# Kernel optimization log

Hardware: AMD Instinct MI355X
Metric: run time of the kernel (lower is better)

## Reference

```python
import math
import jax, jax.numpy as jnp
from jax import lax
import numpy as np

HIDDEN = 128
KQ_CH = HIDDEN * 3  # 384
H, W = 48, 64
N = 4


def _conv(x, w, pad, dil):
    # NCHW conv, OIHW weights, stride 1
    return lax.conv_general_dilated(
        x, w, window_strides=(1, 1),
        padding=[(pad, pad), (pad, pad)],
        rhs_dilation=(dil, dil),
        dimension_numbers=("NCHW", "OIHW", "NCHW"))


def _lrelu(x):
    return jnp.where(x >= 0, x, 0.2 * x)


def setup_inputs() -> dict:
    key = jax.random.key(0)
    ks = jax.random.split(key, 7)
    s = 0.05
    return {
        "k": jax.random.normal(ks[0], (N, KQ_CH, H, W), jnp.float32),
        "q": jax.random.normal(ks[1], (N, KQ_CH, H, W), jnp.float32),
        "v": jax.random.normal(ks[2], (N, HIDDEN, H, W), jnp.float32),
        "w_value": jax.random.normal(ks[3], (HIDDEN, HIDDEN, 1, 1), jnp.float32) * s,
        "w_out": jax.random.normal(ks[4], (HIDDEN, HIDDEN, 3, 3), jnp.float32) * s,
        "w_ff1": jax.random.normal(ks[5], (HIDDEN, HIDDEN, 3, 3), jnp.float32) * s,
        "w_ff2": jax.random.normal(ks[6], (HIDDEN, HIDDEN, 3, 3), jnp.float32) * s,
    }


def reference(k, q, v, w_value, w_out, w_ff1, w_ff2):
    n, c, h, w = k.shape  # c = kq_channels
    hw = h * w
    # value embedding: 1x1 conv
    val = _conv(v, w_value, 0, 1)  # [n, hidden, h, w]
    kf = k.reshape(n, c, hw)
    qf = q.reshape(n, c, hw)
    # scores[n, key_pos, query_pos] = k^T q / sqrt(c)
    scores = jnp.einsum("nck,ncq->nkq", kf, qf) / math.sqrt(c)
    # softmax over key positions (torch dim=-2)
    p_attn = jax.nn.softmax(scores, axis=1)  # [n, hw, hw]
    # p_val = value @ p_attn
    p_val = jnp.einsum("ndk,nkq->ndq", val.reshape(n, -1, hw), p_attn)
    p_val = p_val.reshape(v.shape)
    # residual update with output_linear (conv3x3 + LeakyReLU)
    v2 = v + _lrelu(_conv(p_val, w_out, 1, 1))
    # dilated-conv feed forward with residual
    ff = _lrelu(_conv(_lrelu(_conv(v2, w_ff1, 2, 2)), w_ff2, 1, 1))
    return v2 + ff
```

## Files before the change

### kernel.cpp

```cpp
#include <hip/hip_runtime.h>

#define NB  4
#define CKQ 384
#define DH  128
#define HH  48
#define WW  64
#define HW  3072

#define NSPLIT 16
#define KSEG  (HW / NSPLIT)
#define BQ 128
#define BK 32
#define VSP 40
#define PTS 40
#define XROW 136

typedef short bf16x8 __attribute__((ext_vector_type(8)));
typedef short b16x4  __attribute__((ext_vector_type(4)));
typedef float f32x4  __attribute__((ext_vector_type(4)));
typedef long  i64;
typedef long  i64x2 __attribute__((ext_vector_type(2)));
typedef unsigned short u16;
typedef unsigned int   u32;
typedef unsigned char  u8;
typedef unsigned long long u64;

__device__ __forceinline__ float b2f(u16 u){
  union { u32 i; float f; } x; x.i = ((u32)u) << 16; return x.f;
}
__device__ __forceinline__ u16 f2b(float f){
  union { float f; u32 i; } x; x.f = f;
  u32 r = (x.i + 0x7fffu + ((x.i >> 16) & 1u)) >> 16;
  return (u16)r;
}
__device__ __forceinline__ u8 f2f8(float f){
  return (u8)(__builtin_amdgcn_cvt_pk_fp8_f32(f, f, 0, false) & 0xff);
}

__global__ __launch_bounds__(256)
void tcast8(const float* __restrict__ kin, const float* __restrict__ qin,
            u8* __restrict__ kt8, u8* __restrict__ qt8){
  __shared__ u8 T[64][392];
  const int yy = blockIdx.y;
  const float* in = (yy < NB) ? kin : qin;
  u8* out         = (yy < NB) ? kt8 : qt8;
  const int n  = yy & (NB - 1);
  const int p0 = blockIdx.x * 64;
  const int tx = threadIdx.x & 63;
  const int ty = threadIdx.x >> 6;
  const float* ib = in + (size_t)n * CKQ * HW + p0;
  #pragma unroll 4
  for (int c = ty; c < CKQ; c += 4)
    T[tx][c] = f2f8(ib[(size_t)c * HW + tx]);
  __syncthreads();
  u8* ob = out + ((size_t)n * HW + p0) * CKQ;
  #pragma unroll
  for (int it = 0; it < 12; ++it){
    int ch  = it * 256 + threadIdx.x;
    int row = ch / 48;
    int g   = ch - row * 48;
    *(u64*)(ob + (size_t)row * CKQ + g * 8) = *(const u64*)&T[row][g * 8];
  }
}

__global__ __launch_bounds__(256)
void wprep3(const float* __restrict__ w0, const float* __restrict__ w1,
            const float* __restrict__ w2, u16* __restrict__ o0,
            u16* __restrict__ o1, u16* __restrict__ o2){
  const float* w = (blockIdx.y == 0) ? w0 : (blockIdx.y == 1) ? w1 : w2;
  u16* wt        = (blockIdx.y == 0) ? o0 : (blockIdx.y == 1) ? o1 : o2;
  int g    = blockIdx.x * 256 + threadIdx.x;
  int fid  = g >> 6;
  int lane = g & 63;
  int l15  = lane & 15, quad = lane >> 4;
  int tap  = fid >> 5;
  int cst  = (fid >> 3) & 3;
  int dt   = fid & 7;
  int d    = dt * 16 + l15;
  u16* dst = wt + (size_t)fid * 512 + lane * 8;
  #pragma unroll
  for (int e = 0; e < 8; ++e){
    int c = cst * 32 + quad * 8 + e;
    dst[e] = f2b(w[((size_t)d * DH + c) * 9 + tap]);
  }
}

__global__ __launch_bounds__(256)
void val_embed8(const float* __restrict__ v, const float* __restrict__ wv,
                u8* __restrict__ val8){
  int p  = blockIdx.x * 256 + threadIdx.x;
  int d0 = blockIdx.y * 4;
  int n  = blockIdx.z;
  const float* vb = v + (size_t)n * DH * HW;
  float a0 = 0.f, a1 = 0.f, a2 = 0.f, a3 = 0.f;
  for (int c = 0; c < DH; ++c){
    float vv = vb[c * HW + p];
    a0 += wv[(d0 + 0) * DH + c] * vv;
    a1 += wv[(d0 + 1) * DH + c] * vv;
    a2 += wv[(d0 + 2) * DH + c] * vv;
    a3 += wv[(d0 + 3) * DH + c] * vv;
  }
  u8* ob = val8 + (size_t)n * DH * HW;
  ob[(d0 + 0) * HW + p] = f2f8(a0);
  ob[(d0 + 1) * HW + p] = f2f8(a1);
  ob[(d0 + 2) * HW + p] = f2f8(a2);
  ob[(d0 + 3) * HW + p] = f2f8(a3);
}

__global__ __launch_bounds__(256, 3)
void attn8(const u8* __restrict__ kt, const u8* __restrict__ qt,
           const u8* __restrict__ val, u16* __restrict__ outp,
           float* __restrict__ lsum){
  __shared__ u8 Ks[BK * CKQ];
  __shared__ u8 Vs[DH * VSP];
  __shared__ u8 Pt[BQ * PTS];

  const int tid  = threadIdx.x;
  const int wv   = tid >> 6;
  const int lane = tid & 63;
  const int quad = lane >> 4;
  const int l15  = lane & 15;
  const int n    = blockIdx.z;
  const int seg  = blockIdx.y;
  const int j0   = blockIdx.x * BQ;
  const int jra  = wv * 32 + l15;
  const int jrb  = jra + 16;
  const int ja   = j0 + jra;
  const int jb   = j0 + jrb;

  const u8* qrowa = qt + ((size_t)n * HW + ja) * CKQ;
  const u8* qrowb = qt + ((size_t)n * HW + jb) * CKQ;
  i64 qfa[12], qfb[12];
  #pragma unroll
  for (int cs = 0; cs < 12; ++cs){
    qfa[cs] = *(const i64*)&qrowa[cs * 32 + quad * 8];
    qfb[cs] = *(const i64*)&qrowb[cs * 32 + quad * 8];
  }

  const f32x4 zero = {0.f, 0.f, 0.f, 0.f};
  f32x4 oa[8], obacc[8];
  #pragma unroll
  for (int i = 0; i < 8; ++i){ oa[i] = zero; obacc[i] = zero; }
  float la = 0.f, lbv = 0.f;

  const u8* ktb = kt  + (size_t)n * CKQ * HW;
  const u8* vb  = val + (size_t)n * DH * HW;
  const float scale = 0.05103103630798287f;

  for (int it = 0; it < KSEG / BK; ++it){
    const int i0 = seg * KSEG + it * BK;
    for (int idx = tid; idx < BK * 24; idx += 256){
      int i  = idx / 24;
      int g2 = idx % 24;
      i64x2 dv = *(const i64x2*)&ktb[(size_t)(i0 + i) * CKQ + g2 * 16];
      int g0 = 2 * g2, g1 = g0 + 1;
      int gs0 = (g0 & ~7) | ((g0 ^ i) & 7);
      int gs1 = (g1 & ~7) | ((g1 ^ i) & 7);
      *(i64*)&Ks[i * CKQ + gs0 * 8] = dv[0];
      *(i64*)&Ks[i * CKQ + gs1 * 8] = dv[1];
    }
    for (int idx = tid; idx < DH * 4; idx += 256){
      int dd = idx >> 2;
      int c8 = idx & 3;
      *(i64*)&Vs[dd * VSP + c8 * 8] = *(const i64*)&vb[(size_t)dd * HW + i0 + c8 * 8];
    }
    __syncthreads();

    f32x4 s0a = zero, s1a = zero, s0b = zero, s1b = zero;
    #pragma unroll
    for (int cs = 0; cs < 12; ++cs){
      int g  = 4 * cs + quad;
      int gs = (g & ~7) | ((g ^ l15) & 7);
      i64 a0 = *(const i64*)&Ks[l15 * CKQ + gs * 8];
      i64 a1 = *(const i64*)&Ks[(16 + l15) * CKQ + gs * 8];
      s0a = __builtin_amdgcn_mfma_f32_16x16x32_fp8_fp8(a0, qfa[cs], s0a, 0, 0, 0);
      s1a = __builtin_amdgcn_mfma_f32_16x16x32_fp8_fp8(a1, qfa[cs], s1a, 0, 0, 0);
      s0b = __builtin_amdgcn_mfma_f32_16x16x32_fp8_fp8(a0, qfb[cs], s0b, 0, 0, 0);
      s1b = __builtin_amdgcn_mfma_f32_16x16x32_fp8_fp8(a1, qfb[cs], s1b, 0, 0, 0);
    }

    float pa[8], pb[8]; float tsa = 0.f, tsb = 0.f;
    #pragma unroll
    for (int r = 0; r < 4; ++r){
      pa[r]     = __expf(s0a[r] * scale);
      pa[4 + r] = __expf(s1a[r] * scale);
      pb[r]     = __expf(s0b[r] * scale);
      pb[4 + r] = __expf(s1b[r] * scale);
    }
    #pragma unroll
    for (int i = 0; i < 8; ++i){ tsa += pa[i]; tsb += pb[i]; }
    la += tsa; lbv += tsb;

    u32 wa0 = __builtin_amdgcn_cvt_pk_fp8_f32(pa[0], pa[1], 0, false);
    wa0     = __builtin_amdgcn_cvt_pk_fp8_f32(pa[2], pa[3], wa0, true);
    u32 wa1 = __builtin_amdgcn_cvt_pk_fp8_f32(pa[4], pa[5], 0, false);
    wa1     = __builtin_amdgcn_cvt_pk_fp8_f32(pa[6], pa[7], wa1, true);
    u32 wb0 = __builtin_amdgcn_cvt_pk_fp8_f32(pb[0], pb[1], 0, false);
    wb0     = __builtin_amdgcn_cvt_pk_fp8_f32(pb[2], pb[3], wb0, true);
    u32 wb1 = __builtin_amdgcn_cvt_pk_fp8_f32(pb[4], pb[5], 0, false);
    wb1     = __builtin_amdgcn_cvt_pk_fp8_f32(pb[6], pb[7], wb1, true);
    *(u32*)&Pt[jra * PTS + quad * 4]      = wa0;
    *(u32*)&Pt[jra * PTS + 16 + quad * 4] = wa1;
    *(u32*)&Pt[jrb * PTS + quad * 4]      = wb0;
    *(u32*)&Pt[jrb * PTS + 16 + quad * 4] = wb1;
    __builtin_amdgcn_wave_barrier();

    i64 bpa = *(const i64*)&Pt[jra * PTS + quad * 8];
    i64 bpb = *(const i64*)&Pt[jrb * PTS + quad * 8];
    #pragma unroll
    for (int dt = 0; dt < 8; ++dt){
      i64 av = *(const i64*)&Vs[(dt * 16 + l15) * VSP + quad * 8];
      oa[dt]    = __builtin_amdgcn_mfma_f32_16x16x32_fp8_fp8(av, bpa, oa[dt], 0, 0, 0);
      obacc[dt] = __builtin_amdgcn_mfma_f32_16x16x32_fp8_fp8(av, bpb, obacc[dt], 0, 0, 0);
    }
    __syncthreads();
  }

  la  += __shfl_xor(la, 16);  la  += __shfl_xor(la, 32);
  lbv += __shfl_xor(lbv, 16); lbv += __shfl_xor(lbv, 32);

  u16* obp = outp + ((size_t)(seg * NB + n) * HW) * DH;
  #pragma unroll
  for (int dt = 0; dt < 8; ++dt){
    b16x4 pka = { (short)f2b(oa[dt][0]), (short)f2b(oa[dt][1]),
                  (short)f2b(oa[dt][2]), (short)f2b(oa[dt][3]) };
    b16x4 pkb = { (short)f2b(obacc[dt][0]), (short)f2b(obacc[dt][1]),
                  (short)f2b(obacc[dt][2]), (short)f2b(obacc[dt][3]) };
    *(b16x4*)&obp[(size_t)ja * DH + dt * 16 + quad * 4] = pka;
    *(b16x4*)&obp[(size_t)jb * DH + dt * 16 + quad * 4] = pkb;
  }
  if (quad == 0){
    lsum[(size_t)(seg * NB + n) * HW + ja] = la;
    lsum[(size_t)(seg * NB + n) * HW + jb] = lbv;
  }
}

__global__ __launch_bounds__(256)
void combine(const u16* __restrict__ ob, const float* __restrict__ lb,
             u16* __restrict__ pval_t){
  size_t flat = (size_t)blockIdx.x * 256 + threadIdx.x;
  int d = (int)(flat & 127);
  size_t nj = flat >> 7;
  int j = (int)(nj % HW);
  int n = (int)(nj / HW);
  float acc = 0.f, ls = 0.f;
  #pragma unroll
  for (int s = 0; s < NSPLIT; ++s){
    acc += b2f(ob[((size_t)(s * NB + n) * HW + j) * DH + d]);
    ls  += lb[(size_t)(s * NB + n) * HW + j];
  }
  pval_t[flat] = f2b(acc / ls);
}

template<int DIL, int RESM, int OUTM>
__global__ __launch_bounds__(256, 3)
void mconv(const u16* __restrict__ in_t, const u16* __restrict__ wtf,
           const void* __restrict__ res, void* __restrict__ out){
  __shared__ u16 Xs[3 * 64 * XROW];

  const int tid  = threadIdx.x;
  const int w    = tid >> 6;
  const int lane = tid & 63;
  const int quad = lane >> 4;
  const int l15  = lane & 15;
  const int n    = blockIdx.z;
  const int y    = blockIdx.x;
  const int by   = blockIdx.y;
  const int xw   = w * 16;

  const bf16x8 bz8 = {0,0,0,0,0,0,0,0};
  #pragma unroll
  for (int yi = 0; yi < 3; ++yi){
    int ysrc = y + (yi - 1) * DIL;
    bool ok = (unsigned)ysrc < (unsigned)HH;
    #pragma unroll
    for (int pass = 0; pass < 4; ++pass){
      int ch = pass * 256 + tid;
      int x  = ch >> 4;
      int g  = ch & 15;
      bf16x8 v = bz8;
      if (ok)
        v = *(const bf16x8*)&in_t[((size_t)n * HW + ysrc * WW + x) * DH + g * 8];
      *(bf16x8*)&Xs[(yi * 64 + x) * XROW + g * 8] = v;
    }
  }
  __syncthreads();

  f32x4 acc[2];
  acc[0] = (f32x4){0.f, 0.f, 0.f, 0.f};
  acc[1] = (f32x4){0.f, 0.f, 0.f, 0.f};

  #pragma unroll
  for (int tap = 0; tap < 9; ++tap){
    const int yi = tap / 3;
    const int dx = (tap % 3 - 1) * DIL;
    const int xp = xw + l15 + dx;
    const bool vx = (unsigned)xp < (unsigned)WW;
    const int xc = vx ? xp : 0;
    const u16* xrow = &Xs[(yi * 64 + xc) * XROW];
    #pragma unroll
    for (int cst = 0; cst < 4; ++cst){
      bf16x8 bf = bz8;
      if (vx) bf = *(const bf16x8*)&xrow[cst * 32 + quad * 8];
      #pragma unroll
      for (int dt = 0; dt < 2; ++dt){
        int fid = (tap * 4 + cst) * 8 + by * 2 + dt;
        bf16x8 af = *(const bf16x8*)&wtf[(size_t)fid * 512 + lane * 8];
        acc[dt] = __builtin_amdgcn_mfma_f32_16x16x32_bf16(af, bf, acc[dt], 0, 0, 0);
      }
    }
  }

  const int p = y * WW + xw + l15;
  #pragma unroll
  for (int dt = 0; dt < 2; ++dt){
    const int d0q = by * 32 + dt * 16 + quad * 4;
    float v4[4];
    #pragma unroll
    for (int r = 0; r < 4; ++r){
      float vv = acc[dt][r];
      vv = (vv >= 0.f) ? vv : 0.2f * vv;
      if (RESM == 1)
        vv += ((const float*)res)[((size_t)n * DH + d0q + r) * HW + p];
      v4[r] = vv;
    }
    if (RESM == 2){
      b16x4 rv = *(const b16x4*)&((const u16*)res)[((size_t)n * HW + p) * DH + d0q];
      #pragma unroll
      for (int r = 0; r < 4; ++r) v4[r] += b2f((u16)rv[r]);
    }
    if (OUTM == 0){
      b16x4 pk = { (short)f2b(v4[0]), (short)f2b(v4[1]),
                   (short)f2b(v4[2]), (short)f2b(v4[3]) };
      *(b16x4*)&((u16*)out)[((size_t)n * HW + p) * DH + d0q] = pk;
    } else {
      #pragma unroll
      for (int r = 0; r < 4; ++r)
        ((float*)out)[((size_t)n * DH + d0q + r) * HW + p] = v4[r];
    }
  }
}

extern "C" void kernel_launch(void* const* d_in, const int* in_sizes, int n_in,
                              void* d_out, int out_size, void* d_ws, size_t ws_size,
                              hipStream_t stream){
  const float* k    = (const float*)d_in[0];
  const float* q    = (const float*)d_in[1];
  const float* v    = (const float*)d_in[2];
  const float* wv   = (const float*)d_in[3];
  const float* wout = (const float*)d_in[4];
  const float* wff1 = (const float*)d_in[5];
  const float* wff2 = (const float*)d_in[6];
  float* out = (float*)d_out;

  const size_t TEN  = (size_t)NB * DH * HW;
  const size_t KTEN = (size_t)NB * CKQ * HW;
  const size_t WT   = (size_t)9 * DH * DH;
  u8*  kt8    = (u8*)d_ws;
  u8*  qt8    = kt8 + KTEN;
  u8*  val8   = qt8 + KTEN;
  u16* wt1    = (u16*)(val8 + TEN);
  u16* wt2    = wt1 + WT;
  u16* wt3    = wt2 + WT;
  u16* pval_t = wt3 + WT;
  u16* v2_t   = pval_t + TEN;
  u16* tmid_t = v2_t + TEN;
  u16* ob     = tmid_t + TEN;
  float* lb   = (float*)(ob + (size_t)NSPLIT * TEN);

  tcast8    <<<dim3(48, 2 * NB), 256, 0, stream>>>(k, q, kt8, qt8);
  wprep3    <<<dim3(72, 3), 256, 0, stream>>>(wout, wff1, wff2, wt1, wt2, wt3);
  val_embed8<<<dim3(12, 32, NB), 256, 0, stream>>>(v, wv, val8);
  attn8     <<<dim3(HW / BQ, NSPLIT, NB), 256, 0, stream>>>(kt8, qt8, val8, ob, lb);
  combine   <<<dim3((unsigned)(TEN / 256)), 256, 0, stream>>>(ob, lb, pval_t);
  mconv<1, 1, 0><<<dim3(48, 4, NB), 256, 0, stream>>>(pval_t, wt1, (const void*)v,    (void*)v2_t);
  mconv<2, 0, 0><<<dim3(48, 4, NB), 256, 0, stream>>>(v2_t,   wt2, (const void*)nullptr, (void*)tmid_t);
  mconv<1, 2, 1><<<dim3(48, 4, NB), 256, 0, stream>>>(tmid_t, wt3, (const void*)v2_t, (void*)out);
}
```

Measured before the change: 231.9 us.

## Merge prep kernels into one launch and split attention launch in two halves

Fuses the fp8 transpose-cast, weight repacking and value embedding into one prep kernel dispatched by block index, cutting two launches. The value embedding now computes 16 output channels per thread instead of 4, so each input load is reused across more channels. The attention kernel now takes a segment offset and is launched twice with half the split each. That halves the grid per launch but adds one launch, plausibly to affect scheduling or cache behaviour.

```diff
diff --git a/kernel.cpp b/kernel.cpp
--- a/kernel.cpp
+++ b/kernel.cpp
@@ -38,79 +38,86 @@
 }
 
 __global__ __launch_bounds__(256)
-void tcast8(const float* __restrict__ kin, const float* __restrict__ qin,
-            u8* __restrict__ kt8, u8* __restrict__ qt8){
+void prep(const float* __restrict__ k, const float* __restrict__ q,
+          const float* __restrict__ v, const float* __restrict__ wv,
+          const float* __restrict__ w0, const float* __restrict__ w1,
+          const float* __restrict__ w2,
+          u8* __restrict__ kt8, u8* __restrict__ qt8, u8* __restrict__ val8,
+          u16* __restrict__ o0, u16* __restrict__ o1, u16* __restrict__ o2){
   __shared__ u8 T[64][392];
-  const int yy = blockIdx.y;
-  const float* in = (yy < NB) ? kin : qin;
-  u8* out         = (yy < NB) ? kt8 : qt8;
-  const int n  = yy & (NB - 1);
-  const int p0 = blockIdx.x * 64;
-  const int tx = threadIdx.x & 63;
-  const int ty = threadIdx.x >> 6;
-  const float* ib = in + (size_t)n * CKQ * HW + p0;
-  #pragma unroll 4
-  for (int c = ty; c < CKQ; c += 4)
-    T[tx][c] = f2f8(ib[(size_t)c * HW + tx]);
-  __syncthreads();
-  u8* ob = out + ((size_t)n * HW + p0) * CKQ;
-  #pragma unroll
-  for (int it = 0; it < 12; ++it){
-    int ch  = it * 256 + threadIdx.x;
-    int row = ch / 48;
-    int g   = ch - row * 48;
-    *(u64*)(ob + (size_t)row * CKQ + g * 8) = *(const u64*)&T[row][g * 8];
-  }
-}
-
-__global__ __launch_bounds__(256)
-void wprep3(const float* __restrict__ w0, const float* __restrict__ w1,
-            const float* __restrict__ w2, u16* __restrict__ o0,
-            u16* __restrict__ o1, u16* __restrict__ o2){
-  const float* w = (blockIdx.y == 0) ? w0 : (blockIdx.y == 1) ? w1 : w2;
-  u16* wt        = (blockIdx.y == 0) ? o0 : (blockIdx.y == 1) ? o1 : o2;
-  int g    = blockIdx.x * 256 + threadIdx.x;
-  int fid  = g >> 6;
-  int lane = g & 63;
-  int l15  = lane & 15, quad = lane >> 4;
-  int tap  = fid >> 5;
-  int cst  = (fid >> 3) & 3;
-  int dt   = fid & 7;
-  int d    = dt * 16 + l15;
-  u16* dst = wt + (size_t)fid * 512 + lane * 8;
-  #pragma unroll
-  for (int e = 0; e < 8; ++e){
-    int c = cst * 32 + quad * 8 + e;
-    dst[e] = f2b(w[((size_t)d * DH + c) * 9 + tap]);
-  }
-}
-
-__global__ __launch_bounds__(256)
-void val_embed8(const float* __restrict__ v, const float* __restrict__ wv,
-                u8* __restrict__ val8){
-  int p  = blockIdx.x * 256 + threadIdx.x;
-  int d0 = blockIdx.y * 4;
-  int n  = blockIdx.z;
-  const float* vb = v + (size_t)n * DH * HW;
-  float a0 = 0.f, a1 = 0.f, a2 = 0.f, a3 = 0.f;
-  for (int c = 0; c < DH; ++c){
-    float vv = vb[c * HW + p];
-    a0 += wv[(d0 + 0) * DH + c] * vv;
-    a1 += wv[(d0 + 1) * DH + c] * vv;
-    a2 += wv[(d0 + 2) * DH + c] * vv;
-    a3 += wv[(d0 + 3) * DH + c] * vv;
-  }
-  u8* ob = val8 + (size_t)n * DH * HW;
-  ob[(d0 + 0) * HW + p] = f2f8(a0);
-  ob[(d0 + 1) * HW + p] = f2f8(a1);
-  ob[(d0 + 2) * HW + p] = f2f8(a2);
-  ob[(d0 + 3) * HW + p] = f2f8(a3);
+  const int b   = blockIdx.x;
+  const int tid = threadIdx.x;
+
+  if (b < 384){
+    const int yy = b / 48;
+    const int bx = b % 48;
+    const float* in = (yy < NB) ? k : q;
+    u8* outp        = (yy < NB) ? kt8 : qt8;
+    const int n  = yy & (NB - 1);
+    const int p0 = bx * 64;
+    const int tx = tid & 63;
+    const int ty = tid >> 6;
+    const float* ib = in + (size_t)n * CKQ * HW + p0;
+    #pragma unroll 4
+    for (int c = ty; c < CKQ; c += 4)
+      T[tx][c] = f2f8(ib[(size_t)c * HW + tx]);
+    __syncthreads();
+    u8* ob = outp + ((size_t)n * HW + p0) * CKQ;
+    #pragma unroll
+    for (int it = 0; it < 12; ++it){
+      int ch  = it * 256 + tid;
+      int row = ch / 48;
+      int g   = ch - row * 48;
+      *(u64*)(ob + (size_t)row * CKQ + g * 8) = *(const u64*)&T[row][g * 8];
+    }
+  } else if (b < 600){
+    const int bb = b - 384;
+    const int bx = bb % 72;
+    const int wy = bb / 72;
+    const float* w = (wy == 0) ? w0 : (wy == 1) ? w1 : w2;
+    u16* wt        = (wy == 0) ? o0 : (wy == 1) ? o1 : o2;
+    int g    = bx * 256 + tid;
+    int fid  = g >> 6;
+    int lane = g & 63;
+    int l15  = lane & 15, quad = lane >> 4;
+    int tap  = fid >> 5;
+    int cst  = (fid >> 3) & 3;
+    int dt   = fid & 7;
+    int d    = dt * 16 + l15;
+    u16* dst = wt + (size_t)fid * 512 + lane * 8;
+    #pragma unroll
+    for (int e = 0; e < 8; ++e){
+      int c = cst * 32 + quad * 8 + e;
+      dst[e] = f2b(w[((size_t)d * DH + c) * 9 + tap]);
+    }
+  } else {
+    const int bb = b - 600;
+    const int px = bb % 12;
+    const int db = (bb / 12) & 7;
+    const int n  = bb / 96;
+    const int p  = px * 256 + tid;
+    const int d0 = db * 16;
+    const float* vb = v + (size_t)n * DH * HW;
+    float acc[16];
+    #pragma unroll
+    for (int dd = 0; dd < 16; ++dd) acc[dd] = 0.f;
+    for (int c = 0; c < DH; ++c){
+      float vv = vb[(size_t)c * HW + p];
+      #pragma unroll
+      for (int dd = 0; dd < 16; ++dd)
+        acc[dd] += wv[(d0 + dd) * DH + c] * vv;
+    }
+    u8* ob = val8 + (size_t)n * DH * HW;
+    #pragma unroll
+    for (int dd = 0; dd < 16; ++dd)
+      ob[(size_t)(d0 + dd) * HW + p] = f2f8(acc[dd]);
+  }
 }
 
 __global__ __launch_bounds__(256, 3)
 void attn8(const u8* __restrict__ kt, const u8* __restrict__ qt,
            const u8* __restrict__ val, u16* __restrict__ outp,
-           float* __restrict__ lsum){
+           float* __restrict__ lsum, int seg0){
   __shared__ u8 Ks[BK * CKQ];
   __shared__ u8 Vs[DH * VSP];
   __shared__ u8 Pt[BQ * PTS];
@@ -121,7 +128,7 @@
   const int quad = lane >> 4;
   const int l15  = lane & 15;
   const int n    = blockIdx.z;
-  const int seg  = blockIdx.y;
+  const int seg  = seg0 + blockIdx.y;
   const int j0   = blockIdx.x * BQ;
   const int jra  = wv * 32 + l15;
   const int jrb  = jra + 16;
@@ -278,10 +285,10 @@
       int ch = pass * 256 + tid;
       int x  = ch >> 4;
       int g  = ch & 15;
-      bf16x8 v = bz8;
+      bf16x8 vv = bz8;
       if (ok)
-        v = *(const bf16x8*)&in_t[((size_t)n * HW + ysrc * WW + x) * DH + g * 8];
-      *(bf16x8*)&Xs[(yi * 64 + x) * XROW + g * 8] = v;
+        vv = *(const bf16x8*)&in_t[((size_t)n * HW + ysrc * WW + x) * DH + g * 8];
+      *(bf16x8*)&Xs[(yi * 64 + x) * XROW + g * 8] = vv;
     }
   }
   __syncthreads();
@@ -368,11 +375,11 @@
   u16* ob     = tmid_t + TEN;
   float* lb   = (float*)(ob + (size_t)NSPLIT * TEN);
 
-  tcast8    <<<dim3(48, 2 * NB), 256, 0, stream>>>(k, q, kt8, qt8);
-  wprep3    <<<dim3(72, 3), 256, 0, stream>>>(wout, wff1, wff2, wt1, wt2, wt3);
-  val_embed8<<<dim3(12, 32, NB), 256, 0, stream>>>(v, wv, val8);
-  attn8     <<<dim3(HW / BQ, NSPLIT, NB), 256, 0, stream>>>(kt8, qt8, val8, ob, lb);
-  combine   <<<dim3((unsigned)(TEN / 256)), 256, 0, stream>>>(ob, lb, pval_t);
+  prep   <<<dim3(984), 256, 0, stream>>>(k, q, v, wv, wout, wff1, wff2,
+                                         kt8, qt8, val8, wt1, wt2, wt3);
+  attn8  <<<dim3(HW / BQ, NSPLIT / 2, NB), 256, 0, stream>>>(kt8, qt8, val8, ob, lb, 0);
+  attn8  <<<dim3(HW / BQ, NSPLIT / 2, NB), 256, 0, stream>>>(kt8, qt8, val8, ob, lb, NSPLIT / 2);
+  combine<<<dim3((unsigned)(TEN / 256)), 256, 0, stream>>>(ob, lb, pval_t);
   mconv<1, 1, 0><<<dim3(48, 4, NB), 256, 0, stream>>>(pval_t, wt1, (const void*)v,    (void*)v2_t);
   mconv<2, 0, 0><<<dim3(48, 4, NB), 256, 0, stream>>>(v2_t,   wt2, (const void*)nullptr, (void*)tmid_t);
   mconv<1, 2, 1><<<dim3(48, 4, NB), 256, 0, stream>>>(tmid_t, wt3, (const void*)v2_t, (void*)out);
```

After: 232.0 us. About the same (+0.1%).
